# Kernel tuning notes

Measured on AMD Instinct MI355X. Metric: run time of the kernel, lower is better.

Reference implementation:

```python
import jax, jax.numpy as jnp
import numpy as np

LAMBDA_ATTENTION = 0.33
LAMBDA_DISTANCE = 0.33
LAMBDA_ADJACENCY = 1.0 - LAMBDA_ATTENTION - LAMBDA_DISTANCE
EPS = 1e-06
NEG_INF = 1000000000000.0


def setup_inputs() -> dict:
    key = jax.random.key(0)
    kq, kk, kv, ka, kd = jax.random.split(key, 5)
    B, H, S, D = 16, 16, 512, 64
    return {
        "query": jax.random.normal(kq, (B, H, S, D), dtype=jnp.float32),
        "key": jax.random.normal(kk, (B, H, S, D), dtype=jnp.float32),
        "value": jax.random.normal(kv, (B, H, S, D), dtype=jnp.float32),
        "mask": jnp.ones((B, 1, S), dtype=jnp.float32),
        "adj_matrix": jax.random.uniform(ka, (B, S, S), dtype=jnp.float32),
        "distance_matrix": jax.random.uniform(kd, (B, S, S), dtype=jnp.float32),
    }


def reference(query, key, value, mask, adj_matrix, distance_matrix):
    d_k = query.shape[-1]
    # scores: [B,H,S,S]
    scores = jnp.einsum("bhqd,bhkd->bhqk", query, key) / jnp.sqrt(jnp.asarray(d_k, query.dtype))
    # mask [B,1,S] -> broadcast to [B,H,S,S] over key axis
    key_mask = mask[:, :, None, :]  # [B,1,1,S]
    scores = jnp.where(key_mask == 0, -NEG_INF, scores)
    p_attn = jax.nn.softmax(scores, axis=-1)

    # row-normalized adjacency, broadcast over heads
    adj_norm = adj_matrix / (jnp.sum(adj_matrix, axis=-1, keepdims=True) + EPS)  # [B,S,S]

    # distance kernel: mask key positions with +inf then softmax(-x)
    dist = jnp.where(mask == 0, jnp.inf, distance_matrix)  # mask [B,1,S] broadcasts over rows
    p_dist = jax.nn.softmax(-dist, axis=-1)  # [B,S,S]

    p_weighted = (LAMBDA_ATTENTION * p_attn
                  + LAMBDA_DISTANCE * p_dist[:, None, :, :]
                  + LAMBDA_ADJACENCY * adj_norm[:, None, :, :])
    # dropout is identity in eval mode
    out = jnp.einsum("bhqk,bhkd->bhqd", p_weighted, value)
    return out, p_attn
```

## Files before the change

kernel.cpp:

```cpp
#include <hip/hip_runtime.h>
#include <cmath>

#define BATCH 16
#define HEADS 16
#define SEQ   512
#define DIM   64
#define QT    32
#define NCHUNK 8

#define LAMBDA_A 0.33f
#define LAMBDA_D 0.33f
#define LAMBDA_J 0.34f
#define NEG_BIG  1.0e12f

typedef float  floatx4 __attribute__((ext_vector_type(4)));
typedef short  shortx8 __attribute__((ext_vector_type(8)));
typedef short  shortx4 __attribute__((ext_vector_type(4)));

__device__ __forceinline__ unsigned short f2bf(float x){
  unsigned u = __builtin_bit_cast(unsigned, x);
  u += 0x7FFFu + ((u >> 16) & 1u);
  return (unsigned short)(u >> 16);
}

__global__ __launch_bounds__(256, 8) void prep_w_kernel(
    const float* __restrict__ adj, const float* __restrict__ dist,
    const float* __restrict__ mask, float* __restrict__ W)
{
  int tid  = threadIdx.x;
  int lane = tid & 63;
  int row  = blockIdx.x * 4 + (tid >> 6);
  int b = row >> 9, q = row & (SEQ - 1);
  const float* arow = adj  + ((size_t)b * SEQ + q) * SEQ;
  const float* drow = dist + ((size_t)b * SEQ + q) * SEQ;
  const float* mrow = mask + (size_t)b * SEQ;

  floatx4 a[2], e[2];
  float asum = 0.f, dsum = 0.f;
#pragma unroll
  for (int i = 0; i < 2; i++){
    int c4 = (i * 64 + lane) * 4;
    a[i] = *(const floatx4*)(arow + c4);
    floatx4 d4 = *(const floatx4*)(drow + c4);
    floatx4 m4 = *(const floatx4*)(mrow + c4);
#pragma unroll
    for (int j = 0; j < 4; j++){
      asum += a[i][j];
      float ex = (m4[j] == 0.f) ? 0.f : __expf(-d4[j]);
      e[i][j] = ex;
      dsum += ex;
    }
  }
#pragma unroll
  for (int off = 1; off < 64; off <<= 1){
    asum += __shfl_xor(asum, off);
    dsum += __shfl_xor(dsum, off);
  }
  float ia = LAMBDA_J / (asum + 1e-6f);
  float id = LAMBDA_D / dsum;

  float* wrow = W + ((size_t)b * SEQ + q) * SEQ;
#pragma unroll
  for (int i = 0; i < 2; i++){
    int c4 = (i * 64 + lane) * 4;
    floatx4 w;
#pragma unroll
    for (int j = 0; j < 4; j++) w[j] = e[i][j] * id + a[i][j] * ia;
    *(floatx4*)(wrow + c4) = w;
  }
}

__global__ __launch_bounds__(256, 8) void prep_kvt_kernel(
    const float* __restrict__ K, const float* __restrict__ V,
    unsigned short* __restrict__ Kb, unsigned short* __restrict__ VTb)
{
  int tid = threadIdx.x;
  int c   = blockIdx.x & 7;
  int bh  = blockIdx.x >> 3;
  const float* Kp = K + ((size_t)bh * SEQ + c * 64) * DIM;
  const float* Vp = V + ((size_t)bh * SEQ + c * 64) * DIM;
  unsigned short* Ko = Kb  + ((size_t)bh * SEQ + c * 64) * DIM;
  unsigned short* Vo = VTb + (size_t)bh * DIM * SEQ;

  __shared__ unsigned short sT[64 * 72];

#pragma unroll
  for (int i = 0; i < 2; i++){
    int idx = (i * 256 + tid) * 8;
    floatx4 v0 = *(const floatx4*)(Kp + idx);
    floatx4 v1 = *(const floatx4*)(Kp + idx + 4);
    shortx8 hh;
#pragma unroll
    for (int j = 0; j < 4; j++){
      hh[j]     = (short)f2bf(v0[j]);
      hh[j + 4] = (short)f2bf(v1[j]);
    }
    *(shortx8*)(Ko + idx) = hh;
  }

#pragma unroll
  for (int i = 0; i < 4; i++){
    int idx = (i * 256 + tid) * 4;
    int k = idx >> 6, d = idx & 63;
    floatx4 v = *(const floatx4*)(Vp + idx);
#pragma unroll
    for (int j = 0; j < 4; j++) sT[(d + j) * 72 + k] = f2bf(v[j]);
  }
  __syncthreads();
#pragma unroll
  for (int i = 0; i < 2; i++){
    int idx = i * 256 + tid;
    int d = idx >> 3, k8 = idx & 7;
    shortx8 hh = *(const shortx8*)&sT[d * 72 + k8 * 8];
    *(shortx8*)(Vo + (size_t)d * SEQ + c * 64 + k8 * 8) = hh;
  }
}

__global__ __launch_bounds__(256, 4) void attn_kernel(
    const float* __restrict__ Q, const unsigned short* __restrict__ Kb,
    const unsigned short* __restrict__ VTb, const float* __restrict__ mask,
    const float* __restrict__ W, float* __restrict__ out, float* __restrict__ pattn)
{
  int bx  = blockIdx.x;
  int h   = bx & 15;
  int rest= bx >> 4;
  int qt  = rest & 15;
  int b   = rest >> 4;
  int bh  = b * HEADS + h;
  int q0  = qt * QT;

  int tid  = threadIdx.x;
  int wave = tid >> 6;
  int lane = tid & 63;
  int l15  = lane & 15;
  int quad = lane >> 4;
  int mtile = wave & 1;
  int p     = wave >> 1;

  __shared__ float sMask[SEQ];
  __shared__ unsigned short sPW[2][32 * 72];
  __shared__ float sRedM[2][32];
  __shared__ float sRedS[2][32];

  sMask[tid]       = mask[b * SEQ + tid];
  sMask[tid + 256] = mask[b * SEQ + tid + 256];

  const float* Qb = Q + ((size_t)bh * SEQ + q0 + mtile * 16 + l15) * DIM;
  shortx8 af[2];
#pragma unroll
  for (int ks = 0; ks < 2; ks++){
    const float* qp = Qb + ks * 32 + quad * 8;
    floatx4 v0 = *(const floatx4*)qp;
    floatx4 v1 = *(const floatx4*)(qp + 4);
#pragma unroll
    for (int j = 0; j < 4; j++){
      af[ks][j]     = (short)f2bf(v0[j] * 0.125f);
      af[ks][j + 4] = (short)f2bf(v1[j] * 0.125f);
    }
  }
  __syncthreads();

  const unsigned short* Kw = Kb + (size_t)bh * SEQ * DIM
                               + (size_t)(p * 16 + l15) * DIM + quad * 8;
  floatx4 acc[16];
#pragma unroll
  for (int j = 0; j < 16; j++) acc[j] = (floatx4)0.f;
#pragma unroll
  for (int cc = 0; cc < NCHUNK; cc++){
    const unsigned short* Kc = Kw + cc * 64 * DIM;
#pragma unroll
    for (int ks = 0; ks < 2; ks++){
      shortx8 b0 = *(const shortx8*)(Kc + ks * 32);
      acc[2 * cc]     = __builtin_amdgcn_mfma_f32_16x16x32_bf16(af[ks], b0, acc[2 * cc], 0, 0, 0);
      shortx8 b1 = *(const shortx8*)(Kc + 32 * DIM + ks * 32);
      acc[2 * cc + 1] = __builtin_amdgcn_mfma_f32_16x16x32_bf16(af[ks], b1, acc[2 * cc + 1], 0, 0, 0);
    }
  }

  float vmax[4] = {-INFINITY, -INFINITY, -INFINITY, -INFINITY};
#pragma unroll
  for (int j = 0; j < 16; j++){
    int n = (2 * j + p) * 16 + l15;
    bool msk0 = (sMask[n] == 0.f);
#pragma unroll
    for (int r = 0; r < 4; r++){
      float s = msk0 ? -NEG_BIG : acc[j][r];
      acc[j][r] = s;
      vmax[r] = fmaxf(vmax[r], s);
    }
  }
#pragma unroll
  for (int r = 0; r < 4; r++){
#pragma unroll
    for (int off = 1; off < 16; off <<= 1)
      vmax[r] = fmaxf(vmax[r], __shfl_xor(vmax[r], off));
  }
  if (l15 == 0){
#pragma unroll
    for (int r = 0; r < 4; r++) sRedM[p][mtile * 16 + quad * 4 + r] = vmax[r];
  }
  __syncthreads();
  float mrow[4];
#pragma unroll
  for (int r = 0; r < 4; r++){
    int ridx = mtile * 16 + quad * 4 + r;
    mrow[r] = fmaxf(sRedM[0][ridx], sRedM[1][ridx]);
  }
  float vsum[4] = {0.f, 0.f, 0.f, 0.f};
#pragma unroll
  for (int j = 0; j < 16; j++){
#pragma unroll
    for (int r = 0; r < 4; r++){
      float e = __expf(acc[j][r] - mrow[r]);
      acc[j][r] = e;
      vsum[r] += e;
    }
  }
#pragma unroll
  for (int r = 0; r < 4; r++){
#pragma unroll
    for (int off = 1; off < 16; off <<= 1)
      vsum[r] += __shfl_xor(vsum[r], off);
  }
  if (l15 == 0){
#pragma unroll
    for (int r = 0; r < 4; r++) sRedS[p][mtile * 16 + quad * 4 + r] = vsum[r];
  }
  __syncthreads();
  float inv_l[4];
#pragma unroll
  for (int r = 0; r < 4; r++){
    int ridx = mtile * 16 + quad * 4 + r;
    inv_l[r] = 1.f / (sRedS[0][ridx] + sRedS[1][ridx]);
  }

  float* pA = pattn + ((size_t)bh * SEQ + q0) * SEQ;
  const float* Wq = W + ((size_t)b * SEQ + q0) * SEQ;
  const unsigned short* Vw = VTb + (size_t)bh * DIM * SEQ
                                 + (size_t)(p * 16 + l15) * SEQ + quad * 8;

  floatx4 acc2[2];
  acc2[0] = (floatx4)0.f;
  acc2[1] = (floatx4)0.f;

  float wreg[4][2];
#pragma unroll
  for (int r = 0; r < 4; r++){
    int rl = mtile * 16 + quad * 4 + r;
#pragma unroll
    for (int jj = 0; jj < 2; jj++){
      int nloc = (2 * jj + p) * 16 + l15;
      wreg[r][jj] = Wq[(size_t)rl * SEQ + nloc];
    }
  }

#pragma unroll
  for (int cc = 0; cc < NCHUNK; cc++){
    int buf = cc & 1;
    shortx8 vt0[2], vt1[2];
#pragma unroll
    for (int ks = 0; ks < 2; ks++){
      vt0[ks] = *(const shortx8*)(Vw + cc * 64 + ks * 32);
      vt1[ks] = *(const shortx8*)(Vw + (size_t)32 * SEQ + cc * 64 + ks * 32);
    }
#pragma unroll
    for (int r = 0; r < 4; r++){
      int rl = mtile * 16 + quad * 4 + r;
#pragma unroll
      for (int jj = 0; jj < 2; jj++){
        int nloc = (2 * jj + p) * 16 + l15;
        int n    = cc * 64 + nloc;
        float pa = acc[2 * cc + jj][r] * inv_l[r];
        __builtin_nontemporal_store(pa, &pA[(size_t)rl * SEQ + n]);
        float pw = LAMBDA_A * pa + wreg[r][jj];
        sPW[buf][rl * 72 + nloc] = f2bf(pw);
      }
    }
    int cn = (cc + 1) & 7;
#pragma unroll
    for (int r = 0; r < 4; r++){
      int rl = mtile * 16 + quad * 4 + r;
#pragma unroll
      for (int jj = 0; jj < 2; jj++){
        int nloc = (2 * jj + p) * 16 + l15;
        wreg[r][jj] = Wq[(size_t)rl * SEQ + cn * 64 + nloc];
      }
    }
    __syncthreads();
#pragma unroll
    for (int ks = 0; ks < 2; ks++){
      shortx8 a2 = *(const shortx8*)&sPW[buf][(mtile * 16 + l15) * 72 + ks * 32 + quad * 8];
      acc2[0] = __builtin_amdgcn_mfma_f32_16x16x32_bf16(a2, vt0[ks], acc2[0], 0, 0, 0);
      acc2[1] = __builtin_amdgcn_mfma_f32_16x16x32_bf16(a2, vt1[ks], acc2[1], 0, 0, 0);
    }
  }

  float* ob = out + ((size_t)bh * SEQ + q0) * DIM;
#pragma unroll
  for (int t = 0; t < 2; t++){
    int nt = p + 2 * t;
#pragma unroll
    for (int r = 0; r < 4; r++){
      int rl = mtile * 16 + quad * 4 + r;
      __builtin_nontemporal_store(acc2[t][r], &ob[(size_t)rl * DIM + nt * 16 + l15]);
    }
  }
}

extern "C" void kernel_launch(void* const* d_in, const int* in_sizes, int n_in,
                              void* d_out, int out_size, void* d_ws, size_t ws_size,
                              hipStream_t stream){
  const float* Q    = (const float*)d_in[0];
  const float* K    = (const float*)d_in[1];
  const float* V    = (const float*)d_in[2];
  const float* mask = (const float*)d_in[3];
  const float* adj  = (const float*)d_in[4];
  const float* dist = (const float*)d_in[5];
  float* out   = (float*)d_out;
  float* pattn = out + (size_t)BATCH * HEADS * SEQ * DIM;

  float*          Wbuf = (float*)d_ws;
  unsigned short* Kb   = (unsigned short*)((char*)d_ws + (size_t)16 * 1024 * 1024);
  unsigned short* VTb  = (unsigned short*)((char*)d_ws + (size_t)32 * 1024 * 1024);

  prep_w_kernel  <<<BATCH * SEQ / 4,            256, 0, stream>>>(adj, dist, mask, Wbuf);
  prep_kvt_kernel<<<BATCH * HEADS * NCHUNK,     256, 0, stream>>>(K, V, Kb, VTb);
  attn_kernel    <<<BATCH * HEADS * (SEQ / QT), 256, 0, stream>>>(Q, Kb, VTb, mask, Wbuf,
                                                                  out, pattn);
}
```

Before: 510.3 us.

## Fuse prep kernels and give each wave full 16-row attention rows

The two prep kernels are merged into one launch that splits on block index. The attention kernel is restructured so each wave owns 16 query rows across all 512 keys, computing S^T via swapped MFMA operands. Softmax reductions then stay inside the wave, which removes the shared-memory reductions and block barriers, and p_attn is written as float4 vector stores. The cost is many more accumulator registers per wave (32 floatx4), which lowers occupancy to 2 blocks per CU and risks spills.

```diff
diff --git a/kernel.cpp b/kernel.cpp
--- a/kernel.cpp
+++ b/kernel.cpp
@@ -5,8 +5,6 @@
 #define HEADS 16
 #define SEQ   512
 #define DIM   64
-#define QT    32
-#define NCHUNK 8
 
 #define LAMBDA_A 0.33f
 #define LAMBDA_D 0.33f
@@ -23,66 +21,66 @@
   return (unsigned short)(u >> 16);
 }
 
-__global__ __launch_bounds__(256, 8) void prep_w_kernel(
+__global__ __launch_bounds__(256, 8) void prep_kernel(
     const float* __restrict__ adj, const float* __restrict__ dist,
-    const float* __restrict__ mask, float* __restrict__ W)
-{
-  int tid  = threadIdx.x;
-  int lane = tid & 63;
-  int row  = blockIdx.x * 4 + (tid >> 6);
-  int b = row >> 9, q = row & (SEQ - 1);
-  const float* arow = adj  + ((size_t)b * SEQ + q) * SEQ;
-  const float* drow = dist + ((size_t)b * SEQ + q) * SEQ;
-  const float* mrow = mask + (size_t)b * SEQ;
-
-  floatx4 a[2], e[2];
-  float asum = 0.f, dsum = 0.f;
-#pragma unroll
-  for (int i = 0; i < 2; i++){
-    int c4 = (i * 64 + lane) * 4;
-    a[i] = *(const floatx4*)(arow + c4);
-    floatx4 d4 = *(const floatx4*)(drow + c4);
-    floatx4 m4 = *(const floatx4*)(mrow + c4);
-#pragma unroll
-    for (int j = 0; j < 4; j++){
-      asum += a[i][j];
-      float ex = (m4[j] == 0.f) ? 0.f : __expf(-d4[j]);
-      e[i][j] = ex;
-      dsum += ex;
-    }
-  }
-#pragma unroll
-  for (int off = 1; off < 64; off <<= 1){
-    asum += __shfl_xor(asum, off);
-    dsum += __shfl_xor(dsum, off);
-  }
-  float ia = LAMBDA_J / (asum + 1e-6f);
-  float id = LAMBDA_D / dsum;
-
-  float* wrow = W + ((size_t)b * SEQ + q) * SEQ;
-#pragma unroll
-  for (int i = 0; i < 2; i++){
-    int c4 = (i * 64 + lane) * 4;
-    floatx4 w;
-#pragma unroll
-    for (int j = 0; j < 4; j++) w[j] = e[i][j] * id + a[i][j] * ia;
-    *(floatx4*)(wrow + c4) = w;
-  }
-}
-
-__global__ __launch_bounds__(256, 8) void prep_kvt_kernel(
-    const float* __restrict__ K, const float* __restrict__ V,
+    const float* __restrict__ mask, const float* __restrict__ K,
+    const float* __restrict__ V, float* __restrict__ W,
     unsigned short* __restrict__ Kb, unsigned short* __restrict__ VTb)
 {
+  __shared__ unsigned short sT[64 * 72];
   int tid = threadIdx.x;
-  int c   = blockIdx.x & 7;
-  int bh  = blockIdx.x >> 3;
+
+  if (blockIdx.x < BATCH * SEQ / 4){
+    int lane = tid & 63;
+    int row  = blockIdx.x * 4 + (tid >> 6);
+    int b = row >> 9, q = row & (SEQ - 1);
+    const float* arow = adj  + ((size_t)b * SEQ + q) * SEQ;
+    const float* drow = dist + ((size_t)b * SEQ + q) * SEQ;
+    const float* mrow = mask + (size_t)b * SEQ;
+
+    floatx4 a[2], e[2];
+    float asum = 0.f, dsum = 0.f;
+#pragma unroll
+    for (int i = 0; i < 2; i++){
+      int c4 = (i * 64 + lane) * 4;
+      a[i] = *(const floatx4*)(arow + c4);
+      floatx4 d4 = *(const floatx4*)(drow + c4);
+      floatx4 m4 = *(const floatx4*)(mrow + c4);
+#pragma unroll
+      for (int j = 0; j < 4; j++){
+        asum += a[i][j];
+        float ex = (m4[j] == 0.f) ? 0.f : __expf(-d4[j]);
+        e[i][j] = ex;
+        dsum += ex;
+      }
+    }
+#pragma unroll
+    for (int off = 1; off < 64; off <<= 1){
+      asum += __shfl_xor(asum, off);
+      dsum += __shfl_xor(dsum, off);
+    }
+    float ia = LAMBDA_J / (asum + 1e-6f);
+    float id = LAMBDA_D / dsum;
+
+    float* wrow = W + ((size_t)b * SEQ + q) * SEQ;
+#pragma unroll
+    for (int i = 0; i < 2; i++){
+      int c4 = (i * 64 + lane) * 4;
+      floatx4 w;
+#pragma unroll
+      for (int j = 0; j < 4; j++) w[j] = e[i][j] * id + a[i][j] * ia;
+      *(floatx4*)(wrow + c4) = w;
+    }
+    return;
+  }
+
+  int bid = blockIdx.x - BATCH * SEQ / 4;
+  int c   = bid & 7;
+  int bh  = bid >> 3;
   const float* Kp = K + ((size_t)bh * SEQ + c * 64) * DIM;
   const float* Vp = V + ((size_t)bh * SEQ + c * 64) * DIM;
   unsigned short* Ko = Kb  + ((size_t)bh * SEQ + c * 64) * DIM;
   unsigned short* Vo = VTb + (size_t)bh * DIM * SEQ;
-
-  __shared__ unsigned short sT[64 * 72];
 
 #pragma unroll
   for (int i = 0; i < 2; i++){
@@ -116,194 +114,138 @@
   }
 }
 
-__global__ __launch_bounds__(256, 4) void attn_kernel(
+__global__ __launch_bounds__(256, 2) void attn_kernel(
     const float* __restrict__ Q, const unsigned short* __restrict__ Kb,
     const unsigned short* __restrict__ VTb, const float* __restrict__ mask,
     const float* __restrict__ W, float* __restrict__ out, float* __restrict__ pattn)
 {
-  int bx  = blockIdx.x;
-  int h   = bx & 15;
-  int rest= bx >> 4;
-  int qt  = rest & 15;
-  int b   = rest >> 4;
-  int bh  = b * HEADS + h;
-  int q0  = qt * QT;
+  int bx = blockIdx.x;
+  int qt = bx & 7;
+  int h  = (bx >> 3) & 15;
+  int b  = bx >> 7;
+  int bh = b * HEADS + h;
 
   int tid  = threadIdx.x;
-  int wave = tid >> 6;
+  int wv   = tid >> 6;
   int lane = tid & 63;
   int l15  = lane & 15;
   int quad = lane >> 4;
-  int mtile = wave & 1;
-  int p     = wave >> 1;
-
-  __shared__ float sMask[SEQ];
-  __shared__ unsigned short sPW[2][32 * 72];
-  __shared__ float sRedM[2][32];
-  __shared__ float sRedS[2][32];
-
-  sMask[tid]       = mask[b * SEQ + tid];
-  sMask[tid + 256] = mask[b * SEQ + tid + 256];
-
-  const float* Qb = Q + ((size_t)bh * SEQ + q0 + mtile * 16 + l15) * DIM;
-  shortx8 af[2];
+  int q0   = qt * 64 + wv * 16;
+
+  __shared__ short sPW[4][16 * 72];
+  short* slab = &sPW[wv][0];
+
+  const float* Qp = Q + ((size_t)bh * SEQ + q0 + l15) * DIM + quad * 8;
+  shortx8 qf[2];
 #pragma unroll
   for (int ks = 0; ks < 2; ks++){
-    const float* qp = Qb + ks * 32 + quad * 8;
-    floatx4 v0 = *(const floatx4*)qp;
-    floatx4 v1 = *(const floatx4*)(qp + 4);
+    floatx4 v0 = *(const floatx4*)(Qp + ks * 32);
+    floatx4 v1 = *(const floatx4*)(Qp + ks * 32 + 4);
 #pragma unroll
     for (int j = 0; j < 4; j++){
-      af[ks][j]     = (short)f2bf(v0[j] * 0.125f);
-      af[ks][j + 4] = (short)f2bf(v1[j] * 0.125f);
-    }
-  }
-  __syncthreads();
+      qf[ks][j]     = (short)f2bf(v0[j] * 0.125f);
+      qf[ks][j + 4] = (short)f2bf(v1[j] * 0.125f);
+    }
+  }
 
   const unsigned short* Kw = Kb + (size_t)bh * SEQ * DIM
-                               + (size_t)(p * 16 + l15) * DIM + quad * 8;
-  floatx4 acc[16];
-#pragma unroll
-  for (int j = 0; j < 16; j++) acc[j] = (floatx4)0.f;
-#pragma unroll
-  for (int cc = 0; cc < NCHUNK; cc++){
-    const unsigned short* Kc = Kw + cc * 64 * DIM;
+                                + (size_t)l15 * DIM + quad * 8;
+  floatx4 acc[32];
+#pragma unroll
+  for (int j = 0; j < 32; j++) acc[j] = (floatx4)0.f;
+#pragma unroll
+  for (int j = 0; j < 32; j++){
+    const unsigned short* Kt = Kw + (size_t)j * 16 * DIM;
+    shortx8 k0 = *(const shortx8*)(Kt);
+    shortx8 k1 = *(const shortx8*)(Kt + 32);
+    acc[j] = __builtin_amdgcn_mfma_f32_16x16x32_bf16(k0, qf[0], acc[j], 0, 0, 0);
+    acc[j] = __builtin_amdgcn_mfma_f32_16x16x32_bf16(k1, qf[1], acc[j], 0, 0, 0);
+  }
+
+  const float* mrow = mask + b * SEQ + quad * 4;
+  float mx = -INFINITY;
+#pragma unroll
+  for (int j = 0; j < 32; j++){
+    floatx4 m4 = *(const floatx4*)(mrow + j * 16);
+#pragma unroll
+    for (int r = 0; r < 4; r++){
+      float s = (m4[r] == 0.f) ? -NEG_BIG : acc[j][r];
+      acc[j][r] = s;
+      mx = fmaxf(mx, s);
+    }
+  }
+  mx = fmaxf(mx, __shfl_xor(mx, 16));
+  mx = fmaxf(mx, __shfl_xor(mx, 32));
+
+  float sm = 0.f;
+#pragma unroll
+  for (int j = 0; j < 32; j++){
+#pragma unroll
+    for (int r = 0; r < 4; r++){
+      float e = __expf(acc[j][r] - mx);
+      acc[j][r] = e;
+      sm += e;
+    }
+  }
+  sm += __shfl_xor(sm, 16);
+  sm += __shfl_xor(sm, 32);
+  float inv_l  = 1.f / sm;
+  float lam_il = LAMBDA_A * inv_l;
+
+  float* pAl = pattn + ((size_t)bh * SEQ + q0 + l15) * SEQ + quad * 4;
+  const float* Wl = W + ((size_t)b * SEQ + q0 + l15) * SEQ + quad * 4;
+  const unsigned short* Vw = VTb + (size_t)bh * DIM * SEQ
+                                 + (size_t)l15 * SEQ + quad * 8;
+
+  floatx4 acc2[4];
+#pragma unroll
+  for (int d = 0; d < 4; d++) acc2[d] = (floatx4)0.f;
+
+  floatx4 wcur[4], wnxt[4];
+#pragma unroll
+  for (int jj = 0; jj < 4; jj++) wcur[jj] = *(const floatx4*)(Wl + jj * 16);
+
+#pragma unroll
+  for (int cc = 0; cc < 8; cc++){
+    if (cc < 7){
+#pragma unroll
+      for (int jj = 0; jj < 4; jj++)
+        wnxt[jj] = *(const floatx4*)(Wl + (cc + 1) * 64 + jj * 16);
+    }
+#pragma unroll
+    for (int jj = 0; jj < 4; jj++){
+      int j = cc * 4 + jj;
+      floatx4 pa;
+      shortx4 pw;
+#pragma unroll
+      for (int r = 0; r < 4; r++){
+        float e = acc[j][r];
+        pa[r] = e * inv_l;
+        pw[r] = (short)f2bf(fmaf(e, lam_il, wcur[jj][r]));
+      }
+      __builtin_nontemporal_store(pa, (floatx4*)(pAl + j * 16));
+      *(shortx4*)&slab[l15 * 72 + jj * 16 + quad * 4] = pw;
+    }
+    const unsigned short* Vc = Vw + cc * 64;
 #pragma unroll
     for (int ks = 0; ks < 2; ks++){
-      shortx8 b0 = *(const shortx8*)(Kc + ks * 32);
-      acc[2 * cc]     = __builtin_amdgcn_mfma_f32_16x16x32_bf16(af[ks], b0, acc[2 * cc], 0, 0, 0);
-      shortx8 b1 = *(const shortx8*)(Kc + 32 * DIM + ks * 32);
-      acc[2 * cc + 1] = __builtin_amdgcn_mfma_f32_16x16x32_bf16(af[ks], b1, acc[2 * cc + 1], 0, 0, 0);
-    }
-  }
-
-  float vmax[4] = {-INFINITY, -INFINITY, -INFINITY, -INFINITY};
-#pragma unroll
-  for (int j = 0; j < 16; j++){
-    int n = (2 * j + p) * 16 + l15;
-    bool msk0 = (sMask[n] == 0.f);
-#pragma unroll
-    for (int r = 0; r < 4; r++){
-      float s = msk0 ? -NEG_BIG : acc[j][r];
-      acc[j][r] = s;
-      vmax[r] = fmaxf(vmax[r], s);
-    }
-  }
-#pragma unroll
-  for (int r = 0; r < 4; r++){
-#pragma unroll
-    for (int off = 1; off < 16; off <<= 1)
-      vmax[r] = fmaxf(vmax[r], __shfl_xor(vmax[r], off));
-  }
-  if (l15 == 0){
-#pragma unroll
-    for (int r = 0; r < 4; r++) sRedM[p][mtile * 16 + quad * 4 + r] = vmax[r];
-  }
-  __syncthreads();
-  float mrow[4];
-#pragma unroll
-  for (int r = 0; r < 4; r++){
-    int ridx = mtile * 16 + quad * 4 + r;
-    mrow[r] = fmaxf(sRedM[0][ridx], sRedM[1][ridx]);
-  }
-  float vsum[4] = {0.f, 0.f, 0.f, 0.f};
-#pragma unroll
-  for (int j = 0; j < 16; j++){
-#pragma unroll
-    for (int r = 0; r < 4; r++){
-      float e = __expf(acc[j][r] - mrow[r]);
-      acc[j][r] = e;
-      vsum[r] += e;
-    }
-  }
-#pragma unroll
-  for (int r = 0; r < 4; r++){
-#pragma unroll
-    for (int off = 1; off < 16; off <<= 1)
-      vsum[r] += __shfl_xor(vsum[r], off);
-  }
-  if (l15 == 0){
-#pragma unroll
-    for (int r = 0; r < 4; r++) sRedS[p][mtile * 16 + quad * 4 + r] = vsum[r];
-  }
-  __syncthreads();
-  float inv_l[4];
-#pragma unroll
-  for (int r = 0; r < 4; r++){
-    int ridx = mtile * 16 + quad * 4 + r;
-    inv_l[r] = 1.f / (sRedS[0][ridx] + sRedS[1][ridx]);
-  }
-
-  float* pA = pattn + ((size_t)bh * SEQ + q0) * SEQ;
-  const float* Wq = W + ((size_t)b * SEQ + q0) * SEQ;
-  const unsigned short* Vw = VTb + (size_t)bh * DIM * SEQ
-                                 + (size_t)(p * 16 + l15) * SEQ + quad * 8;
-
-  floatx4 acc2[2];
-  acc2[0] = (floatx4)0.f;
-  acc2[1] = (floatx4)0.f;
-
-  float wreg[4][2];
-#pragma unroll
-  for (int r = 0; r < 4; r++){
-    int rl = mtile * 16 + quad * 4 + r;
-#pragma unroll
-    for (int jj = 0; jj < 2; jj++){
-      int nloc = (2 * jj + p) * 16 + l15;
-      wreg[r][jj] = Wq[(size_t)rl * SEQ + nloc];
-    }
-  }
-
-#pragma unroll
-  for (int cc = 0; cc < NCHUNK; cc++){
-    int buf = cc & 1;
-    shortx8 vt0[2], vt1[2];
-#pragma unroll
-    for (int ks = 0; ks < 2; ks++){
-      vt0[ks] = *(const shortx8*)(Vw + cc * 64 + ks * 32);
-      vt1[ks] = *(const shortx8*)(Vw + (size_t)32 * SEQ + cc * 64 + ks * 32);
-    }
-#pragma unroll
-    for (int r = 0; r < 4; r++){
-      int rl = mtile * 16 + quad * 4 + r;
-#pragma unroll
-      for (int jj = 0; jj < 2; jj++){
-        int nloc = (2 * jj + p) * 16 + l15;
-        int n    = cc * 64 + nloc;
-        float pa = acc[2 * cc + jj][r] * inv_l[r];
-        __builtin_nontemporal_store(pa, &pA[(size_t)rl * SEQ + n]);
-        float pw = LAMBDA_A * pa + wreg[r][jj];
-        sPW[buf][rl * 72 + nloc] = f2bf(pw);
+      shortx8 a2 = *(const shortx8*)&slab[l15 * 72 + ks * 32 + quad * 8];
+#pragma unroll
+      for (int d = 0; d < 4; d++){
+        shortx8 vf = *(const shortx8*)(Vc + (size_t)d * 16 * SEQ + ks * 32);
+        acc2[d] = __builtin_amdgcn_mfma_f32_16x16x32_bf16(a2, vf, acc2[d], 0, 0, 0);
       }
     }
-    int cn = (cc + 1) & 7;
-#pragma unroll
-    for (int r = 0; r < 4; r++){
-      int rl = mtile * 16 + quad * 4 + r;
-#pragma unroll
-      for (int jj = 0; jj < 2; jj++){
-        int nloc = (2 * jj + p) * 16 + l15;
-        wreg[r][jj] = Wq[(size_t)rl * SEQ + cn * 64 + nloc];
-      }
-    }
-    __syncthreads();
-#pragma unroll
-    for (int ks = 0; ks < 2; ks++){
-      shortx8 a2 = *(const shortx8*)&sPW[buf][(mtile * 16 + l15) * 72 + ks * 32 + quad * 8];
-      acc2[0] = __builtin_amdgcn_mfma_f32_16x16x32_bf16(a2, vt0[ks], acc2[0], 0, 0, 0);
-      acc2[1] = __builtin_amdgcn_mfma_f32_16x16x32_bf16(a2, vt1[ks], acc2[1], 0, 0, 0);
-    }
-  }
-
-  float* ob = out + ((size_t)bh * SEQ + q0) * DIM;
-#pragma unroll
-  for (int t = 0; t < 2; t++){
-    int nt = p + 2 * t;
-#pragma unroll
-    for (int r = 0; r < 4; r++){
-      int rl = mtile * 16 + quad * 4 + r;
-      __builtin_nontemporal_store(acc2[t][r], &ob[(size_t)rl * DIM + nt * 16 + l15]);
-    }
+#pragma unroll
+    for (int jj = 0; jj < 4; jj++) wcur[jj] = wnxt[jj];
+  }
+
+  float* ob = out + ((size_t)bh * SEQ + q0 + quad * 4) * DIM + l15;
+#pragma unroll
+  for (int d = 0; d < 4; d++){
+#pragma unroll
+    for (int r = 0; r < 4; r++)
+      __builtin_nontemporal_store(acc2[d][r], ob + (size_t)r * DIM + d * 16);
   }
 }
 
@@ -323,8 +265,8 @@
   unsigned short* Kb   = (unsigned short*)((char*)d_ws + (size_t)16 * 1024 * 1024);
   unsigned short* VTb  = (unsigned short*)((char*)d_ws + (size_t)32 * 1024 * 1024);
 
-  prep_w_kernel  <<<BATCH * SEQ / 4,            256, 0, stream>>>(adj, dist, mask, Wbuf);
-  prep_kvt_kernel<<<BATCH * HEADS * NCHUNK,     256, 0, stream>>>(K, V, Kb, VTb);
-  attn_kernel    <<<BATCH * HEADS * (SEQ / QT), 256, 0, stream>>>(Q, Kb, VTb, mask, Wbuf,
-                                                                  out, pattn);
-}
+  prep_kernel<<<BATCH * SEQ / 4 + BATCH * HEADS * 8, 256, 0, stream>>>(
+      adj, dist, mask, K, V, Wbuf, Kb, VTb);
+  attn_kernel<<<BATCH * HEADS * (SEQ / 64), 256, 0, stream>>>(
+      Q, Kb, VTb, mask, Wbuf, out, pattn);
+}
```

New measurement: 547.4 us. +7.3%, slower.
